# Kernel tuning notes

Measured on AMD Instinct MI355X. Metric: run time of the kernel, lower is better.

Reference implementation:

```python
import jax, jax.numpy as jnp
import numpy as np

DIM = 512
HEADS = 8
DIM_HEAD = 64
HIDDEN = HEADS * DIM_HEAD  # 512
SCALE = DIM_HEAD ** -0.5


def setup_inputs() -> dict:
    key = jax.random.key(0)
    k1, k2, k3 = jax.random.split(key, 3)
    x = jax.random.normal(k1, (4, 2048, DIM), dtype=jnp.float32)
    # torch Linear weight convention: [out_features, in_features], y = x @ W.T
    W_qkv = jax.random.normal(k2, (3 * HIDDEN, DIM), dtype=jnp.float32) * (DIM ** -0.5)
    W_out = jax.random.normal(k3, (DIM, HIDDEN), dtype=jnp.float32) * (HIDDEN ** -0.5)
    return {"x": x, "W_qkv": W_qkv, "W_out": W_out}


def reference(x, W_qkv, W_out):
    b, n, c = x.shape
    qkv = jnp.einsum('bnc,oc->bno', x, W_qkv)  # [b, n, 3*hidden]
    q, k, v = jnp.split(qkv, 3, axis=-1)
    # rearrange 'b n (h c) -> b h c n'
    def to_heads(t):
        return jnp.transpose(t.reshape(b, n, HEADS, DIM_HEAD), (0, 2, 3, 1))
    q, k, v = to_heads(q), to_heads(k), to_heads(v)
    q = q * SCALE
    sim = jnp.einsum('bhcn,bhcj->bhnj', q, k)  # [b, h, n, n]
    attn = jax.nn.softmax(sim, axis=-1)
    out = jnp.einsum('bhnj,bhdj->bhnd', attn, v)  # [b, h, n, d]
    out = jnp.transpose(out, (0, 2, 1, 3)).reshape(b, n, HIDDEN)  # 'b h n d -> b n (h d)'
    return jnp.einsum('bnh,oh->bno', out, W_out)
```

## Files before the change

kernel.cpp:

```cpp
#include <hip/hip_runtime.h>


typedef unsigned short u16;
typedef __attribute__((ext_vector_type(8))) short s16x8;
typedef __attribute__((ext_vector_type(4))) float f32x4;
typedef __attribute__((ext_vector_type(16))) float f32x16;

__device__ __forceinline__ u16 f2bf(float f) {
  unsigned int u = __float_as_uint(f);
  u = (u + 0x7fffu + ((u >> 16) & 1u)) >> 16;
  return (u16)u;
}

__device__ __forceinline__ void gload16(const u16* g, u16* lds_base) {
  __builtin_amdgcn_global_load_lds(
      (const __attribute__((address_space(1))) unsigned int*)g,
      (__attribute__((address_space(3))) unsigned int*)lds_base, 16, 0, 0);
}

__device__ __forceinline__ void permlane32_swap(unsigned& a, unsigned& b) {
  asm volatile("v_permlane32_swap_b32 %0, %1" : "+v"(a), "+v"(b));
}

__global__ __launch_bounds__(256) void cvt_all(
    const float* __restrict__ x, const float* __restrict__ w1,
    const float* __restrict__ w2, u16* __restrict__ xb,
    u16* __restrict__ w1b, u16* __restrict__ w2b) {
  constexpr int N1 = 8192 * 512 / 4, N2 = 1536 * 512 / 4, N3 = 512 * 512 / 4;
  int i = blockIdx.x * 256 + threadIdx.x;
  if (i >= N1 + N2 + N3) return;
  const float* src;
  u16* dst;
  int j;
  if (i < N1) { src = x; dst = xb; j = i; }
  else if (i < N1 + N2) { src = w1; dst = w1b; j = i - N1; }
  else { src = w2; dst = w2b; j = i - N1 - N2; }
  float4 f = ((const float4*)src)[j];
  uint2 o;
  o.x = (unsigned)f2bf(f.x) | ((unsigned)f2bf(f.y) << 16);
  o.y = (unsigned)f2bf(f.z) | ((unsigned)f2bf(f.w) << 16);
  ((uint2*)dst)[j] = o;
}

template <int BN, int MODE>
__global__ __launch_bounds__(256) void gemm128(
    const u16* __restrict__ A, const u16* __restrict__ B,
    float* __restrict__ Cf,
    u16* __restrict__ Qp, u16* __restrict__ Kp, u16* __restrict__ Vp) {
  constexpr int K = 512;
  constexpr int JN = BN / 32;
  __shared__ u16 smem[128 * 64 + BN * 64];
  u16* As = smem;
  u16* Bs = smem + 128 * 64;
  const int id = blockIdx.x;
  const int bm0 = (id & 63) * 128;
  const int bn0 = (id >> 6) * BN;
  const int t = threadIdx.x, wave = t >> 6, lane = t & 63;
  const int quad = lane >> 4, l16 = lane & 15;
  const int wm = (wave & 1) * 64, wn = (wave >> 1) * (BN / 2);
  const int lr = lane >> 3, lc = lane & 7;
  const int swz = lc ^ lr;

  f32x4 acc[4][JN] = {};

  for (int k0 = 0; k0 < K; k0 += 64) {
    __syncthreads();
#pragma unroll
    for (int a = 0; a < 4; a++) {
      int r = wave * 32 + a * 8 + lr;
      gload16(A + (size_t)(bm0 + r) * K + k0 + swz * 8,
              &As[(wave * 32 + a * 8) * 64]);
    }
#pragma unroll
    for (int b = 0; b < BN / 32; b++) {
      int r = wave * (BN / 4) + b * 8 + lr;
      gload16(B + (size_t)(bn0 + r) * K + k0 + swz * 8,
              &Bs[(wave * (BN / 4) + b * 8) * 64]);
    }
    __syncthreads();
#pragma unroll
    for (int ks = 0; ks < 2; ks++) {
      s16x8 af[4], bf[JN];
#pragma unroll
      for (int i = 0; i < 4; i++) {
        int m = wm + i * 16 + l16;
        af[i] = *(const s16x8*)(&As[m * 64 + (((ks * 4 + quad) ^ (m & 7)) * 8)]);
      }
#pragma unroll
      for (int j = 0; j < JN; j++) {
        int n = wn + j * 16 + l16;
        bf[j] = *(const s16x8*)(&Bs[n * 64 + (((ks * 4 + quad) ^ (n & 7)) * 8)]);
      }
#pragma unroll
      for (int i = 0; i < 4; i++)
#pragma unroll
        for (int j = 0; j < JN; j++)
          acc[i][j] = __builtin_amdgcn_mfma_f32_16x16x32_bf16(af[i], bf[j], acc[i][j], 0, 0, 0);
    }
  }

  if constexpr (MODE == 1) {
#pragma unroll
    for (int i = 0; i < 4; i++)
#pragma unroll
      for (int j = 0; j < JN; j++)
#pragma unroll
        for (int r = 0; r < 4; r++) {
          int m = bm0 + wm + i * 16 + quad * 4 + r;
          int n = bn0 + wn + j * 16 + l16;
          Cf[(size_t)m * 512 + n] = acc[i][j][r];
        }
  } else {
    const int part = bn0 >> 9;
    if (part < 2) {
      const float qs = (part == 0) ? 0.18033688011112042f : 1.0f;
      __syncthreads();
#pragma unroll
      for (int i = 0; i < 4; i++)
#pragma unroll
        for (int j = 0; j < JN; j++)
#pragma unroll
          for (int r = 0; r < 4; r++) {
            int row = wm + i * 16 + quad * 4 + r;
            int cn = wn + j * 16 + l16;
            smem[row * 128 + (((cn >> 3) ^ (row & 7)) << 3) + (cn & 7)] =
                f2bf(acc[i][j][r] * qs);
          }
      __syncthreads();
      u16* dst = (part == 0) ? Qp : Kp;
      const int bb = bm0 >> 11;
      const int tokbase = bm0 & 2047;
      const int headbase = (bn0 & 511) >> 6;
#pragma unroll
      for (int it = 0; it < 8; it++) {
        int row = it * 16 + (t >> 4);
        int n0 = (t & 15) * 8;
        s16x8 pk = *(const s16x8*)(&smem[row * 128 + ((((n0 >> 3) ^ (row & 7))) << 3)]);
        int head = headbase + (n0 >> 6), dh = n0 & 63;
        int tok = tokbase + row;
        *(s16x8*)(&dst[((size_t)(bb * 8 + head) * 2048 + tok) * 64 + dh]) = pk;
      }
    } else {
      __syncthreads();
#pragma unroll
      for (int i = 0; i < 4; i++)
#pragma unroll
        for (int j = 0; j < JN; j++)
#pragma unroll
          for (int r = 0; r < 4; r++) {
            int row = wm + i * 16 + quad * 4 + r;
            int cn = wn + j * 16 + l16;
            smem[row * 128 + (cn ^ (row & 7))] = f2bf(acc[i][j][r]);
          }
      __syncthreads();
      const int bb = bm0 >> 11;
      const int tokbase = bm0 & 2047;
      const int headbase = (bn0 & 511) >> 6;
#pragma unroll
      for (int it = 0; it < 8; it++) {
        int cn = it * 16 + (t >> 4);
        int dh = cn & 63, head = headbase + (cn >> 6);
        int tok0 = (t & 15) * 8;
        s16x8 pk;
#pragma unroll
        for (int k = 0; k < 8; k++) {
          int row = tok0 + k;
          pk[k] = (short)smem[row * 128 + (cn ^ (row & 7))];
        }
        *(s16x8*)(&Vp[((size_t)(bb * 8 + head) * 64 + dh) * 2048 + tokbase + tok0]) = pk;
      }
    }
  }
}

__global__ __launch_bounds__(256) void attn_kernel(
    const u16* __restrict__ Qg, const u16* __restrict__ Kg,
    const u16* __restrict__ Vtg, u16* __restrict__ Og) {
  __shared__ __attribute__((aligned(16))) u16 smem[64 * 72 + 2 * 8 * 520];
  u16* Qs = smem;
  u16* Ks = smem + 64 * 72;
  u16* Vt = Ks + 8 * 520;
  float* Obuf = (float*)smem;
  float* Lbuf = (float*)((char*)smem + 64 * 68 * 4);

  const int id = blockIdx.x;
  const int xcd = id & 7, slot = id >> 3;
  const int bh = xcd * 4 + (slot & 3);
  const int q0 = (slot >> 2) * 64;

  const u16* Qh = Qg + (size_t)bh * 2048 * 64;
  const u16* Kh = Kg + (size_t)bh * 2048 * 64;
  const u16* Vh = Vtg + (size_t)bh * 64 * 2048;
  const int t = threadIdx.x, lane = t & 63, wave = t >> 6;
  const int wq = wave & 1, wk = wave >> 1;
  const int l32 = lane & 31, half = lane >> 5;
  const int srow = t >> 2, scolb = (t & 3) * 8;
  const int lr = lane >> 3, lc = lane & 7, swz = lc ^ lr;
  const int q = wq * 32 + l32;

#pragma unroll
  for (int p = 0; p < 2; p++) {
    int col = scolb + p * 32;
    *(s16x8*)(&Qs[srow * 72 + col]) = *(const s16x8*)(Qh + (size_t)(q0 + srow) * 64 + col);
  }
  __syncthreads();
  s16x8 bQ[4];
#pragma unroll
  for (int ks = 0; ks < 4; ks++)
    bQ[ks] = *(const s16x8*)(&Qs[q * 72 + ks * 16 + half * 8]);

  f32x16 o[2] = {};
  float l_acc = 0.f;

  for (int j0 = 0; j0 < 2048; j0 += 64) {
    __syncthreads();
    {
      int g0 = wave * 2, g1 = wave * 2 + 1;
      gload16(Kh + (size_t)(j0 + g0 * 8 + lr) * 64 + swz * 8, &Ks[g0 * 520]);
      gload16(Kh + (size_t)(j0 + g1 * 8 + lr) * 64 + swz * 8, &Ks[g1 * 520]);
      gload16(Vh + (size_t)(g0 * 8 + lr) * 2048 + j0 + swz * 8, &Vt[g0 * 520]);
      gload16(Vh + (size_t)(g1 * 8 + lr) * 2048 + j0 + swz * 8, &Vt[g1 * 520]);
    }
    __syncthreads();

    f32x16 s = {};
    {
      const int rK = wk * 32 + l32;
      const int base = (rK >> 3) * 520 + (rK & 7) * 64;
#pragma unroll
      for (int ks = 0; ks < 4; ks++) {
        s16x8 aK = *(const s16x8*)(&Ks[base + (((ks * 2 + half) ^ (rK & 7)) * 8)]);
        s = __builtin_amdgcn_mfma_f32_32x32x16_bf16(aK, bQ[ks], s, 0, 0, 0);
      }
    }

    unsigned pu[16];
#pragma unroll
    for (int r = 0; r < 16; r++) {
      float p = __builtin_amdgcn_exp2f(s[r]);
      unsigned u = __float_as_uint(p);
      l_acc += __uint_as_float(u & 0xffff0000u);
      pu[r] = u;
    }
    unsigned g[8];
#pragma unroll
    for (int v = 0; v < 8; v++)
      g[v] = __builtin_amdgcn_perm(pu[2 * v + 1], pu[2 * v], 0x07060302u);
    permlane32_swap(g[0], g[2]);
    permlane32_swap(g[1], g[3]);
    permlane32_swap(g[4], g[6]);
    permlane32_swap(g[5], g[7]);
    s16x8 bP[2];
    ((unsigned*)&bP[0])[0] = g[0]; ((unsigned*)&bP[0])[1] = g[1];
    ((unsigned*)&bP[0])[2] = g[2]; ((unsigned*)&bP[0])[3] = g[3];
    ((unsigned*)&bP[1])[0] = g[4]; ((unsigned*)&bP[1])[1] = g[5];
    ((unsigned*)&bP[1])[2] = g[6]; ((unsigned*)&bP[1])[3] = g[7];

#pragma unroll
    for (int dt = 0; dt < 2; dt++) {
      const int rV = dt * 32 + l32;
      const int base = (rV >> 3) * 520 + (rV & 7) * 64;
#pragma unroll
      for (int s2 = 0; s2 < 2; s2++) {
        s16x8 aV = *(const s16x8*)(&Vt[base + (((wk * 4 + s2 * 2 + half) ^ (rV & 7)) * 8)]);
        o[dt] = __builtin_amdgcn_mfma_f32_32x32x16_bf16(aV, bP[s2], o[dt], 0, 0, 0);
      }
    }
  }

  __syncthreads();
  Lbuf[(wk * 2 + half) * 64 + q] = l_acc;
  if (wk == 1) {
#pragma unroll
    for (int dt = 0; dt < 2; dt++)
#pragma unroll
      for (int gi = 0; gi < 4; gi++) {
        int d0 = 8 * gi + 4 * half + 32 * dt;
        float4 v = { o[dt][4 * gi + 0], o[dt][4 * gi + 1],
                     o[dt][4 * gi + 2], o[dt][4 * gi + 3] };
        *(float4*)(&Obuf[q * 68 + d0]) = v;
      }
  }
  __syncthreads();
  if (wk == 0) {
    float l = Lbuf[0 * 64 + q] + Lbuf[1 * 64 + q] + Lbuf[2 * 64 + q] + Lbuf[3 * 64 + q];
    float sc = __builtin_amdgcn_rcpf(l);
#pragma unroll
    for (int dt = 0; dt < 2; dt++)
#pragma unroll
      for (int gi = 0; gi < 4; gi++) {
        int d0 = 8 * gi + 4 * half + 32 * dt;
        float4 v = *(float4*)(&Obuf[q * 68 + d0]);
        v.x = (v.x + o[dt][4 * gi + 0]) * sc;
        v.y = (v.y + o[dt][4 * gi + 1]) * sc;
        v.z = (v.z + o[dt][4 * gi + 2]) * sc;
        v.w = (v.w + o[dt][4 * gi + 3]) * sc;
        *(float4*)(&Obuf[q * 68 + d0]) = v;
      }
  }
  __syncthreads();

  {
    const int bb = bh >> 3, h = bh & 7;
    int qq = t >> 2, d0 = (t & 3) * 16;
    float f[16];
#pragma unroll
    for (int c = 0; c < 4; c++) {
      float4 v = *(float4*)(&Obuf[qq * 68 + d0 + 4 * c]);
      f[4 * c + 0] = v.x; f[4 * c + 1] = v.y; f[4 * c + 2] = v.z; f[4 * c + 3] = v.w;
    }
    unsigned pk[8];
#pragma unroll
    for (int c = 0; c < 8; c++)
      pk[c] = (unsigned)f2bf(f[2 * c]) | ((unsigned)f2bf(f[2 * c + 1]) << 16);
    size_t base = ((size_t)bb * 2048 + q0 + qq) * 512 + h * 64 + d0;
    uint4 s0 = { pk[0], pk[1], pk[2], pk[3] };
    uint4 s1 = { pk[4], pk[5], pk[6], pk[7] };
    *(uint4*)(&Og[base]) = s0;
    *(uint4*)(&Og[base + 8]) = s1;
  }
}

extern "C" void kernel_launch(void* const* d_in, const int* in_sizes, int n_in,
                              void* d_out, int out_size, void* d_ws, size_t ws_size,
                              hipStream_t stream) {
  const float* x    = (const float*)d_in[0];
  const float* Wqkv = (const float*)d_in[1];
  const float* Wout = (const float*)d_in[2];
  float* y = (float*)d_out;

  char* ws = (char*)d_ws;
  size_t off = 0;
  auto alloc = [&](size_t bytes) {
    void* p = ws + off;
    off += (bytes + 255) & ~(size_t)255;
    return p;
  };
  u16* xb    = (u16*)alloc((size_t)8192 * 512 * 2);
  u16* wqkvb = (u16*)alloc((size_t)1536 * 512 * 2);
  u16* woutb = (u16*)alloc((size_t)512 * 512 * 2);
  u16* Qw    = (u16*)alloc((size_t)32 * 2048 * 64 * 2);
  u16* Kw    = (u16*)alloc((size_t)32 * 2048 * 64 * 2);
  u16* Vw    = (u16*)alloc((size_t)32 * 2048 * 64 * 2);
  u16* Ow    = (u16*)alloc((size_t)8192 * 512 * 2);
  if (off > ws_size) return;

  cvt_all<<<5120, 256, 0, stream>>>(x, Wqkv, Wout, xb, wqkvb, woutb);

  gemm128<128, 0><<<768, 256, 0, stream>>>(xb, wqkvb, nullptr, Qw, Kw, Vw);
  attn_kernel<<<1024, 256, 0, stream>>>(Qw, Kw, Vw, Ow);
  gemm128<64, 1><<<512, 256, 0, stream>>>(Ow, woutb, y, nullptr, nullptr, nullptr);
}
```

Baseline: 161.2 us.

## Double-buffer K/V tiles in LDS to prefetch the next tile during compute

Doubles the LDS staging area so the K and V tiles for iteration j+1 are issued as async global-to-LDS loads while iteration j runs its QK^T, exp and PV MFMAs. The first tile is prefetched before the loop. The two barriers per iteration become one at the end of each step. The aim is to hide global load latency behind matrix work, at the cost of roughly 16 KB more LDS per block, which may reduce how many blocks fit on a CU.

```diff
diff --git a/kernel.cpp b/kernel.cpp
--- a/kernel.cpp
+++ b/kernel.cpp
@@ -176,10 +176,9 @@
 __global__ __launch_bounds__(256) void attn_kernel(
     const u16* __restrict__ Qg, const u16* __restrict__ Kg,
     const u16* __restrict__ Vtg, u16* __restrict__ Og) {
-  __shared__ __attribute__((aligned(16))) u16 smem[64 * 72 + 2 * 8 * 520];
+  __shared__ __attribute__((aligned(16))) u16 smem[64 * 72 + 4 * 8 * 520];
   u16* Qs = smem;
-  u16* Ks = smem + 64 * 72;
-  u16* Vt = Ks + 8 * 520;
+  u16* stage = smem + 64 * 72;
   float* Obuf = (float*)smem;
   float* Lbuf = (float*)((char*)smem + 64 * 68 * 4);
 
@@ -197,13 +196,24 @@
   const int srow = t >> 2, scolb = (t & 3) * 8;
   const int lr = lane >> 3, lc = lane & 7, swz = lc ^ lr;
   const int q = wq * 32 + l32;
+  const int g0 = wave * 2, g1 = wave * 2 + 1;
 
 #pragma unroll
   for (int p = 0; p < 2; p++) {
     int col = scolb + p * 32;
     *(s16x8*)(&Qs[srow * 72 + col]) = *(const s16x8*)(Qh + (size_t)(q0 + srow) * 64 + col);
   }
+
+  {
+    u16* Ks = stage;
+    u16* Vt = stage + 4160;
+    gload16(Kh + (size_t)(g0 * 8 + lr) * 64 + swz * 8, &Ks[g0 * 520]);
+    gload16(Kh + (size_t)(g1 * 8 + lr) * 64 + swz * 8, &Ks[g1 * 520]);
+    gload16(Vh + (size_t)(g0 * 8 + lr) * 2048 + swz * 8, &Vt[g0 * 520]);
+    gload16(Vh + (size_t)(g1 * 8 + lr) * 2048 + swz * 8, &Vt[g1 * 520]);
+  }
   __syncthreads();
+
   s16x8 bQ[4];
 #pragma unroll
   for (int ks = 0; ks < 4; ks++)
@@ -212,16 +222,19 @@
   f32x16 o[2] = {};
   float l_acc = 0.f;
 
-  for (int j0 = 0; j0 < 2048; j0 += 64) {
-    __syncthreads();
-    {
-      int g0 = wave * 2, g1 = wave * 2 + 1;
-      gload16(Kh + (size_t)(j0 + g0 * 8 + lr) * 64 + swz * 8, &Ks[g0 * 520]);
-      gload16(Kh + (size_t)(j0 + g1 * 8 + lr) * 64 + swz * 8, &Ks[g1 * 520]);
-      gload16(Vh + (size_t)(g0 * 8 + lr) * 2048 + j0 + swz * 8, &Vt[g0 * 520]);
-      gload16(Vh + (size_t)(g1 * 8 + lr) * 2048 + j0 + swz * 8, &Vt[g1 * 520]);
-    }
-    __syncthreads();
+  for (int jt = 0; jt < 32; jt++) {
+    const u16* Ks = stage + (jt & 1) * 8320;
+    const u16* Vt = Ks + 4160;
+
+    if (jt < 31) {
+      u16* Kn = stage + ((jt + 1) & 1) * 8320;
+      u16* Vn = Kn + 4160;
+      const int jn = (jt + 1) * 64;
+      gload16(Kh + (size_t)(jn + g0 * 8 + lr) * 64 + swz * 8, &Kn[g0 * 520]);
+      gload16(Kh + (size_t)(jn + g1 * 8 + lr) * 64 + swz * 8, &Kn[g1 * 520]);
+      gload16(Vh + (size_t)(g0 * 8 + lr) * 2048 + jn + swz * 8, &Vn[g0 * 520]);
+      gload16(Vh + (size_t)(g1 * 8 + lr) * 2048 + jn + swz * 8, &Vn[g1 * 520]);
+    }
 
     f32x16 s = {};
     {
@@ -266,9 +279,10 @@
         o[dt] = __builtin_amdgcn_mfma_f32_32x32x16_bf16(aV, bP[s2], o[dt], 0, 0, 0);
       }
     }
-  }
-
-  __syncthreads();
+
+    __syncthreads();
+  }
+
   Lbuf[(wk * 2 + half) * 64 + q] = l_acc;
   if (wk == 1) {
 #pragma unroll
```

Result: no change. 162.0 us (+0.5%).

## Double-buffer GEMM LDS tiles and shrink M tile to 64 for more blocks

Applied to the files above, without the earlier changes.

Replaces the single-buffered GEMM with a double-buffered version that issues global-to-LDS loads for the next K tile while computing the current one, removing one barrier per iteration. The block tile changes to 64x128, doubling the grid for the QKV projection and reshaping the output projection grid. This aims to hide load latency and improve occupancy, at the cost of more LDS per block and less per-block data reuse.

```diff
diff --git a/kernel.cpp b/kernel.cpp
--- a/kernel.cpp
+++ b/kernel.cpp
@@ -42,68 +42,75 @@
   ((uint2*)dst)[j] = o;
 }
 
-template <int BN, int MODE>
-__global__ __launch_bounds__(256) void gemm128(
+template <int MODE>
+__global__ __launch_bounds__(256) void gemm_db(
     const u16* __restrict__ A, const u16* __restrict__ B,
     float* __restrict__ Cf,
     u16* __restrict__ Qp, u16* __restrict__ Kp, u16* __restrict__ Vp) {
   constexpr int K = 512;
-  constexpr int JN = BN / 32;
-  __shared__ u16 smem[128 * 64 + BN * 64];
-  u16* As = smem;
-  u16* Bs = smem + 128 * 64;
+  constexpr int BUF = (64 + 128) * 64;
+  __shared__ u16 smem[2 * BUF];
   const int id = blockIdx.x;
-  const int bm0 = (id & 63) * 128;
-  const int bn0 = (id >> 6) * BN;
+  const int bm0 = (id & 127) * 64;
+  const int bn0 = (id >> 7) * 128;
   const int t = threadIdx.x, wave = t >> 6, lane = t & 63;
   const int quad = lane >> 4, l16 = lane & 15;
-  const int wm = (wave & 1) * 64, wn = (wave >> 1) * (BN / 2);
+  const int wm = (wave & 1) * 32, wn = (wave >> 1) * 64;
   const int lr = lane >> 3, lc = lane & 7;
   const int swz = lc ^ lr;
 
-  f32x4 acc[4][JN] = {};
-
-  for (int k0 = 0; k0 < K; k0 += 64) {
-    __syncthreads();
-#pragma unroll
-    for (int a = 0; a < 4; a++) {
-      int r = wave * 32 + a * 8 + lr;
-      gload16(A + (size_t)(bm0 + r) * K + k0 + swz * 8,
-              &As[(wave * 32 + a * 8) * 64]);
-    }
-#pragma unroll
-    for (int b = 0; b < BN / 32; b++) {
-      int r = wave * (BN / 4) + b * 8 + lr;
-      gload16(B + (size_t)(bn0 + r) * K + k0 + swz * 8,
-              &Bs[(wave * (BN / 4) + b * 8) * 64]);
-    }
-    __syncthreads();
+  f32x4 acc[2][4] = {};
+
+  auto stage = [&](int buf, int kt) {
+    u16* As = smem + buf * BUF;
+    u16* Bs = As + 64 * 64;
+    const int k0 = kt * 64;
+#pragma unroll
+    for (int a = 0; a < 2; a++) {
+      int g = wave * 2 + a;
+      gload16(A + (size_t)(bm0 + g * 8 + lr) * K + k0 + swz * 8, &As[g * 8 * 64]);
+    }
+#pragma unroll
+    for (int b = 0; b < 4; b++) {
+      int g = wave * 4 + b;
+      gload16(B + (size_t)(bn0 + g * 8 + lr) * K + k0 + swz * 8, &Bs[g * 8 * 64]);
+    }
+  };
+
+  stage(0, 0);
+  __syncthreads();
+
+  for (int kt = 0; kt < 8; kt++) {
+    const u16* As = smem + (kt & 1) * BUF;
+    const u16* Bs = As + 64 * 64;
+    if (kt < 7) stage((kt + 1) & 1, kt + 1);
 #pragma unroll
     for (int ks = 0; ks < 2; ks++) {
-      s16x8 af[4], bf[JN];
-#pragma unroll
-      for (int i = 0; i < 4; i++) {
+      s16x8 af[2], bf[4];
+#pragma unroll
+      for (int i = 0; i < 2; i++) {
         int m = wm + i * 16 + l16;
         af[i] = *(const s16x8*)(&As[m * 64 + (((ks * 4 + quad) ^ (m & 7)) * 8)]);
       }
 #pragma unroll
-      for (int j = 0; j < JN; j++) {
+      for (int j = 0; j < 4; j++) {
         int n = wn + j * 16 + l16;
         bf[j] = *(const s16x8*)(&Bs[n * 64 + (((ks * 4 + quad) ^ (n & 7)) * 8)]);
       }
 #pragma unroll
-      for (int i = 0; i < 4; i++)
-#pragma unroll
-        for (int j = 0; j < JN; j++)
+      for (int i = 0; i < 2; i++)
+#pragma unroll
+        for (int j = 0; j < 4; j++)
           acc[i][j] = __builtin_amdgcn_mfma_f32_16x16x32_bf16(af[i], bf[j], acc[i][j], 0, 0, 0);
     }
+    __syncthreads();
   }
 
   if constexpr (MODE == 1) {
 #pragma unroll
-    for (int i = 0; i < 4; i++)
-#pragma unroll
-      for (int j = 0; j < JN; j++)
+    for (int i = 0; i < 2; i++)
+#pragma unroll
+      for (int j = 0; j < 4; j++)
 #pragma unroll
         for (int r = 0; r < 4; r++) {
           int m = bm0 + wm + i * 16 + quad * 4 + r;
@@ -112,13 +119,15 @@
         }
   } else {
     const int part = bn0 >> 9;
+    const int bb = bm0 >> 11;
+    const int tokbase = bm0 & 2047;
+    const int headbase = (bn0 & 511) >> 6;
     if (part < 2) {
       const float qs = (part == 0) ? 0.18033688011112042f : 1.0f;
-      __syncthreads();
-#pragma unroll
-      for (int i = 0; i < 4; i++)
-#pragma unroll
-        for (int j = 0; j < JN; j++)
+#pragma unroll
+      for (int i = 0; i < 2; i++)
+#pragma unroll
+        for (int j = 0; j < 4; j++)
 #pragma unroll
           for (int r = 0; r < 4; r++) {
             int row = wm + i * 16 + quad * 4 + r;
@@ -128,11 +137,8 @@
           }
       __syncthreads();
       u16* dst = (part == 0) ? Qp : Kp;
-      const int bb = bm0 >> 11;
-      const int tokbase = bm0 & 2047;
-      const int headbase = (bn0 & 511) >> 6;
-#pragma unroll
-      for (int it = 0; it < 8; it++) {
+#pragma unroll
+      for (int it = 0; it < 4; it++) {
         int row = it * 16 + (t >> 4);
         int n0 = (t & 15) * 8;
         s16x8 pk = *(const s16x8*)(&smem[row * 128 + ((((n0 >> 3) ^ (row & 7))) << 3)]);
@@ -141,11 +147,10 @@
         *(s16x8*)(&dst[((size_t)(bb * 8 + head) * 2048 + tok) * 64 + dh]) = pk;
       }
     } else {
-      __syncthreads();
-#pragma unroll
-      for (int i = 0; i < 4; i++)
-#pragma unroll
-        for (int j = 0; j < JN; j++)
+#pragma unroll
+      for (int i = 0; i < 2; i++)
+#pragma unroll
+        for (int j = 0; j < 4; j++)
 #pragma unroll
           for (int r = 0; r < 4; r++) {
             int row = wm + i * 16 + quad * 4 + r;
@@ -153,14 +158,11 @@
             smem[row * 128 + (cn ^ (row & 7))] = f2bf(acc[i][j][r]);
           }
       __syncthreads();
-      const int bb = bm0 >> 11;
-      const int tokbase = bm0 & 2047;
-      const int headbase = (bn0 & 511) >> 6;
-#pragma unroll
-      for (int it = 0; it < 8; it++) {
-        int cn = it * 16 + (t >> 4);
+#pragma unroll
+      for (int it = 0; it < 4; it++) {
+        int cn = it * 32 + (t >> 3);
         int dh = cn & 63, head = headbase + (cn >> 6);
-        int tok0 = (t & 15) * 8;
+        int tok0 = (t & 7) * 8;
         s16x8 pk;
 #pragma unroll
         for (int k = 0; k < 8; k++) {
@@ -347,7 +349,7 @@
 
   cvt_all<<<5120, 256, 0, stream>>>(x, Wqkv, Wout, xb, wqkvb, woutb);
 
-  gemm128<128, 0><<<768, 256, 0, stream>>>(xb, wqkvb, nullptr, Qw, Kw, Vw);
+  gemm_db<0><<<1536, 256, 0, stream>>>(xb, wqkvb, nullptr, Qw, Kw, Vw);
   attn_kernel<<<1024, 256, 0, stream>>>(Qw, Kw, Vw, Ow);
-  gemm128<64, 1><<<512, 256, 0, stream>>>(Ow, woutb, y, nullptr, nullptr, nullptr);
-}
+  gemm_db<1><<<512, 256, 0, stream>>>(Ow, woutb, y, nullptr, nullptr, nullptr);
+}
```

New measurement: 149.5 us. 7.2% less time.
